# Optimization experiments

Hardware: AMD Instinct MI355X
Metric: run time of the kernel (lower is better)

Reference implementation:

```python
import jax, jax.numpy as jnp
import numpy as np

B, T, E = 2, 4096, 768
H = 12
WIN = 256  # one-sided window w; band width = 2w+1


def setup_inputs() -> dict:
    key = jax.random.key(0)
    k1, k2, k3, k4 = jax.random.split(key, 4)
    scale = 1.0 / np.sqrt(E)
    return {
        "x": jax.random.normal(k1, (B, T, E), dtype=jnp.float32),
        "Wq": jax.random.normal(k2, (E, E), dtype=jnp.float32) * scale,
        "Wk": jax.random.normal(k3, (E, E), dtype=jnp.float32) * scale,
        "Wv": jax.random.normal(k4, (E, E), dtype=jnp.float32) * scale,
    }


def reference(x, Wq, Wk, Wv):
    b, t, e = x.shape
    h, w = H, WIN
    s = e // h
    Wb = 2 * w + 1          # band width
    nc = t // w             # number of query chunks of size w

    # projections (nn.Linear, bias=False): y = x @ W^T
    q = (x @ Wq.T).reshape(b, t, h, s) * (1.0 / np.sqrt(s))
    k = (x @ Wk.T).reshape(b, t, h, s)
    v = (x @ Wv.T).reshape(b, t, h, s)

    # overlapping key/value chunks: chunk c covers absolute keys [c*w - w, c*w + 2w)
    pad = [(0, 0), (w, w), (0, 0), (0, 0)]
    kp = jnp.pad(k, pad).reshape(b, nc + 2, w, h, s)
    k3 = jnp.concatenate([kp[:, :-2], kp[:, 1:-1], kp[:, 2:]], axis=2)  # [b,nc,3w,h,s]
    vp = jnp.pad(v, pad).reshape(b, nc + 2, w, h, s)
    v3 = jnp.concatenate([vp[:, :-2], vp[:, 1:-1], vp[:, 2:]], axis=2)  # [b,nc,3w,h,s]

    qc = q.reshape(b, nc, w, h, s)
    scores = jnp.einsum('bcxhd,bcyhd->bhcxy', qc, k3)  # [b,h,nc,w,3w]

    # extract the banded diagonals: band j <-> key index p + j in the 3w window
    idx = jnp.arange(w)[:, None] + jnp.arange(Wb)[None, :]  # [w, 2w+1], values in [0,3w)
    band = jnp.take_along_axis(scores, idx[None, None, None], axis=-1)  # [b,h,nc,w,2w+1]
    band = band.reshape(b, h, t, Wb).transpose(0, 2, 1, 3)  # [b,t,h,2w+1]

    # mask_invalid_locations: key absolute pos = i + j - w must lie in [0, t)
    key_pos = jnp.arange(t)[:, None] + jnp.arange(Wb)[None, :] - w
    invalid = (key_pos < 0) | (key_pos >= t)
    band = jnp.where(invalid[None, :, None, :], -jnp.inf, band)

    probs = jax.nn.softmax(band.astype(jnp.float32), axis=-1).astype(x.dtype)

    # sliding_chunks_matmul_pv: scatter band probs back to the 3w window layout
    pc = probs.transpose(0, 2, 1, 3).reshape(b, h, nc, w, Wb)
    pc_pad = jnp.pad(pc, [(0, 0)] * 4 + [(w - 1, w - 1)])  # last axis len 4w-1
    # full[p, m] = band[p, m - p] for m-p in [0, 2w], else 0
    idx2 = (jnp.arange(3 * w)[None, :] - jnp.arange(w)[:, None]) + (w - 1)  # [w, 3w]
    pfull = jnp.take_along_axis(pc_pad, idx2[None, None, None], axis=-1)  # [b,h,nc,w,3w]

    out = jnp.einsum('bhcpm,bcmhd->bcphd', pfull, v3).reshape(b, t, e)
    return out
```

## Files before the change

kernel.cpp:

```cpp
#include <hip/hip_runtime.h>

#define B_ 2
#define T_ 4096
#define E_ 768
#define H_ 12
#define S_ 64
#define WIN_ 256

typedef unsigned short u16;
typedef unsigned int u32;
typedef __attribute__((ext_vector_type(8))) short bf16x8;
typedef __attribute__((ext_vector_type(4))) short bf16x4;
typedef __attribute__((ext_vector_type(4))) float f32x4;

__device__ __forceinline__ u16 f2bf(float f) {
  u32 u = __float_as_uint(f);
  u += ((u >> 16) & 1u) + 0x7fffu;
  return (u16)(u >> 16);
}

__device__ __forceinline__ u32 cvt_pk_bf16(float lo, float hi) {
  u32 r;
  asm("v_cvt_pk_bf16_f32 %0, %1, %2" : "=v"(r) : "v"(lo), "v"(hi));
  return r;
}

__device__ __forceinline__ void async_copy16(const u16* g, u16* l) {
  __builtin_amdgcn_global_load_lds(
      (const __attribute__((address_space(1))) void*)g,
      (__attribute__((address_space(3))) void*)l, 16, 0, 0);
}

__global__ void cvt_all(const float* __restrict__ x, const float* __restrict__ wq,
                        const float* __restrict__ wk, const float* __restrict__ wv,
                        u16* __restrict__ xb, u16* __restrict__ wb) {
  const int n4x = B_ * T_ * E_ / 4;
  const int n4w = E_ * E_ / 4;
  int i = blockIdx.x * 256 + threadIdx.x;
  const float* src;
  u16* dst;
  int j;
  if (i < n4x) {
    src = x; dst = xb; j = i;
  } else {
    int t = i - n4x;
    int z = t / n4w;
    if (z >= 3) return;
    j = t - z * n4w;
    src = (z == 0) ? wq : ((z == 1) ? wk : wv);
    dst = wb + (size_t)z * E_ * E_;
  }
  float4 v = ((const float4*)src)[j];
  ushort4 o;
  o.x = f2bf(v.x); o.y = f2bf(v.y); o.z = f2bf(v.z); o.w = f2bf(v.w);
  ((ushort4*)dst)[j] = o;
}

__global__ __launch_bounds__(256)
void gemm_qkv(const u16* __restrict__ xb, const u16* __restrict__ wb,
              u16* __restrict__ qkv) {
  const int M = B_ * T_;
  __shared__ u16 As[3][128][32];
  __shared__ u16 Bs[3][128][32];
  int tid = threadIdx.x;
  int lane = tid & 63, wave = tid >> 6;
  int wr = wave >> 1, wc = wave & 1;
  int q8 = lane >> 4, nl = lane & 15;
  int bm = blockIdx.x * 128, bn = blockIdx.y * 128;
  int z = blockIdx.z;
  const u16* A = xb;
  const u16* Bmat = wb + (size_t)z * E_ * E_;
  u16* C = qkv + (size_t)z * M * E_;
  float scale = (z == 0) ? (0.125f * 1.44269504088896f) : 1.0f;

  int r0 = tid >> 2, c0 = tid & 3;
  int cs = c0 ^ (r0 & 3);
  const u16* ga0 = A + (size_t)(bm + r0) * E_ + cs * 8;
  const u16* ga1 = A + (size_t)(bm + r0 + 64) * E_ + cs * 8;
  const u16* gb0 = Bmat + (size_t)(bn + r0) * E_ + cs * 8;
  const u16* gb1 = Bmat + (size_t)(bn + r0 + 64) * E_ + cs * 8;
  int l0 = tid * 8;
  int l1 = tid * 8 + 2048;

  int swz8 = (q8 ^ (nl & 3)) * 8;

  const int NK = E_ / 32;
#pragma unroll
  for (int p = 0; p < 2; ++p) {
    int koff = p * 32;
    async_copy16(ga0 + koff, &As[p][0][0] + l0);
    async_copy16(ga1 + koff, &As[p][0][0] + l1);
    async_copy16(gb0 + koff, &Bs[p][0][0] + l0);
    async_copy16(gb1 + koff, &Bs[p][0][0] + l1);
  }

  f32x4 acc[4][4] = {};

#define KSTEP(KI, BUF, PBUF)                                                   \
  {                                                                            \
    asm volatile("s_waitcnt vmcnt(4) lgkmcnt(0)" ::: "memory");                \
    __builtin_amdgcn_s_barrier();                                              \
    __builtin_amdgcn_sched_barrier(0);                                         \
    int kp = ((KI) + 2 < NK) ? (KI) + 2 : NK - 1;                              \
    int koff = kp * 32;                                                        \
    async_copy16(ga0 + koff, &As[PBUF][0][0] + l0);                            \
    async_copy16(ga1 + koff, &As[PBUF][0][0] + l1);                            \
    async_copy16(gb0 + koff, &Bs[PBUF][0][0] + l0);                            \
    async_copy16(gb1 + koff, &Bs[PBUF][0][0] + l1);                            \
    bf16x8 af[4], bfr[4];                                                      \
    _Pragma("unroll")                                                          \
    for (int i = 0; i < 4; ++i)                                                \
      af[i] = *(const bf16x8*)&As[BUF][wr * 64 + i * 16 + nl][swz8];           \
    _Pragma("unroll")                                                          \
    for (int i = 0; i < 4; ++i)                                                \
      bfr[i] = *(const bf16x8*)&Bs[BUF][wc * 64 + i * 16 + nl][swz8];          \
    __builtin_amdgcn_s_setprio(1);                                             \
    _Pragma("unroll")                                                          \
    for (int i = 0; i < 4; ++i)                                                \
      _Pragma("unroll")                                                        \
      for (int j2 = 0; j2 < 4; ++j2)                                           \
        acc[i][j2] = __builtin_amdgcn_mfma_f32_16x16x32_bf16(af[i], bfr[j2],   \
                                                             acc[i][j2], 0, 0, 0); \
    __builtin_amdgcn_s_setprio(0);                                             \
  }

  for (int kb = 0; kb < NK; kb += 3) {
    KSTEP(kb + 0, 0, 2)
    KSTEP(kb + 1, 1, 0)
    KSTEP(kb + 2, 2, 1)
  }
#undef KSTEP

#pragma unroll
  for (int i = 0; i < 4; ++i)
#pragma unroll
    for (int j2 = 0; j2 < 4; ++j2)
#pragma unroll
      for (int r = 0; r < 4; ++r) {
        int row = bm + wr * 64 + i * 16 + q8 * 4 + r;
        int col = bn + wc * 64 + j2 * 16 + nl;
        C[(size_t)row * E_ + col] = f2bf(acc[i][j2][r] * scale);
      }
}

__global__ void transpose_v(const u16* __restrict__ v, u16* __restrict__ vT) {
  __shared__ u16 lt[64][66];
  int t = threadIdx.x;
  int t0 = blockIdx.x * 64;
  int e0 = blockIdx.y * 64;
  int b = blockIdx.z;
#pragma unroll
  for (int i = 0; i < 2; ++i) {
    int u = t + i * 256;
    int tok = u >> 3, cg = u & 7;
    bf16x8 val = *(const bf16x8*)(v + (size_t)(b * T_ + t0 + tok) * E_ + e0 + cg * 8);
#pragma unroll
    for (int j = 0; j < 8; ++j) lt[tok][cg * 8 + j] = (u16)val[j];
  }
  __syncthreads();
#pragma unroll
  for (int i = 0; i < 2; ++i) {
    int u = t + i * 256;
    int d = u >> 3, ck = u & 7;
    bf16x8 o;
#pragma unroll
    for (int j = 0; j < 8; ++j) o[j] = (short)lt[ck * 8 + j][d];
    *(bf16x8*)(vT + (size_t)(b * E_ + e0 + d) * T_ + t0 + ck * 8) = o;
  }
}

__global__ __launch_bounds__(256)
void attn_kernel(const u16* __restrict__ qkv, const u16* __restrict__ vT,
                 float* __restrict__ out) {
  const int Mtot = B_ * T_;
  const u16* qb = qkv;
  const u16* kb = qkv + (size_t)Mtot * E_;

  int tid = threadIdx.x;
  int lane = tid & 63, wave = tid >> 6;
  int q8 = lane >> 4, nl = lane & 15;
  int qs = blockIdx.x * 128;
  int bh = blockIdx.y;
  int b = bh / H_, h = bh % H_;
  int qw = qs + wave * 32;
  size_t ho = (size_t)h * S_;

  bf16x8 aq[2][2];
#pragma unroll
  for (int mt = 0; mt < 2; ++mt) {
    const u16* qrow = qb + (size_t)(b * T_ + qw + mt * 16 + nl) * E_ + ho;
    aq[mt][0] = *(const bf16x8*)(qrow + q8 * 8);
    aq[mt][1] = *(const bf16x8*)(qrow + 32 + q8 * 8);
  }

  f32x4 O[2][4] = {};
  float lacc[2] = {0.f, 0.f};

  int klo = qw - WIN_; if (klo < 0) klo = 0;
  int khi = qw + 32 + WIN_; if (khi > T_) khi = T_;

  const u16* kbase = kb + (size_t)b * T_ * E_ + ho;
  const u16* vbase = vT + (size_t)b * E_ * T_ + ho * T_;

  int alo = ((((q8 << 1) & 3) << 4) + nl) << 2;
  int ahi = alo + 64;
  bool hint = q8 >= 2;

  bf16x8 bk[2][2];
#pragma unroll
  for (int nt = 0; nt < 2; ++nt) {
    const u16* krow = kbase + (size_t)(klo + nt * 16 + nl) * E_;
    bk[nt][0] = *(const bf16x8*)(krow + q8 * 8);
    bk[nt][1] = *(const bf16x8*)(krow + 32 + q8 * 8);
  }

  for (int kt = klo; kt < khi; kt += 32) {
    bf16x8 bv[4];
#pragma unroll
    for (int dt = 0; dt < 4; ++dt)
      bv[dt] = *(const bf16x8*)(vbase + (size_t)(dt * 16 + nl) * T_ + kt + q8 * 8);

    int ktn = (kt + 32 < khi) ? kt + 32 : kt;
    bf16x8 nbk[2][2];
#pragma unroll
    for (int nt = 0; nt < 2; ++nt) {
      const u16* krow = kbase + (size_t)(ktn + nt * 16 + nl) * E_;
      nbk[nt][0] = *(const bf16x8*)(krow + q8 * 8);
      nbk[nt][1] = *(const bf16x8*)(krow + 32 + q8 * 8);
    }

    f32x4 sc[2][2] = {};
    __builtin_amdgcn_s_setprio(1);
#pragma unroll
    for (int nt = 0; nt < 2; ++nt)
#pragma unroll
      for (int mt = 0; mt < 2; ++mt) {
        sc[mt][nt] = __builtin_amdgcn_mfma_f32_16x16x32_bf16(bk[nt][0], aq[mt][0], sc[mt][nt], 0, 0, 0);
        sc[mt][nt] = __builtin_amdgcn_mfma_f32_16x16x32_bf16(bk[nt][1], aq[mt][1], sc[mt][nt], 0, 0, 0);
      }
    __builtin_amdgcn_s_setprio(0);

    if (kt < qw - 225 || kt > qw + 225) {
#pragma unroll
      for (int mt = 0; mt < 2; ++mt)
#pragma unroll
        for (int nt = 0; nt < 2; ++nt)
#pragma unroll
          for (int r = 0; r < 4; ++r) {
            int qa = qw + mt * 16 + nl;
            int ka = kt + nt * 16 + q8 * 4 + r;
            int d = ka - qa;
            sc[mt][nt][r] = (d < -WIN_ || d > WIN_) ? -1e30f : sc[mt][nt][r];
          }
    }

#pragma unroll
    for (int mt = 0; mt < 2; ++mt) {
      float s = 0.f;
#pragma unroll
      for (int nt = 0; nt < 2; ++nt)
#pragma unroll
        for (int r = 0; r < 4; ++r) {
          float p = exp2f(sc[mt][nt][r]);
          sc[mt][nt][r] = p;
          s += p;
        }
      lacc[mt] += s;
    }

    bf16x8 ap[2];
#pragma unroll
    for (int mt = 0; mt < 2; ++mt) {
      u32 pk00 = cvt_pk_bf16(sc[mt][0][0], sc[mt][0][1]);
      u32 pk01 = cvt_pk_bf16(sc[mt][0][2], sc[mt][0][3]);
      u32 pk10 = cvt_pk_bf16(sc[mt][1][0], sc[mt][1][1]);
      u32 pk11 = cvt_pk_bf16(sc[mt][1][2], sc[mt][1][3]);
      int q0a = __builtin_amdgcn_ds_bpermute(alo, (int)pk00);
      int q0b = __builtin_amdgcn_ds_bpermute(alo, (int)pk10);
      int q1a = __builtin_amdgcn_ds_bpermute(alo, (int)pk01);
      int q1b = __builtin_amdgcn_ds_bpermute(alo, (int)pk11);
      int q2a = __builtin_amdgcn_ds_bpermute(ahi, (int)pk00);
      int q2b = __builtin_amdgcn_ds_bpermute(ahi, (int)pk10);
      int q3a = __builtin_amdgcn_ds_bpermute(ahi, (int)pk01);
      int q3b = __builtin_amdgcn_ds_bpermute(ahi, (int)pk11);
      union { u32 w[4]; bf16x8 v; } u;
      u.w[0] = (u32)(hint ? q0b : q0a);
      u.w[1] = (u32)(hint ? q1b : q1a);
      u.w[2] = (u32)(hint ? q2b : q2a);
      u.w[3] = (u32)(hint ? q3b : q3a);
      ap[mt] = u.v;
    }

    __builtin_amdgcn_s_setprio(1);
#pragma unroll
    for (int dt = 0; dt < 4; ++dt)
#pragma unroll
      for (int mt = 0; mt < 2; ++mt)
        O[mt][dt] = __builtin_amdgcn_mfma_f32_16x16x32_bf16(ap[mt], bv[dt], O[mt][dt], 0, 0, 0);
    __builtin_amdgcn_s_setprio(0);

#pragma unroll
    for (int nt = 0; nt < 2; ++nt) {
      bk[nt][0] = nbk[nt][0];
      bk[nt][1] = nbk[nt][1];
    }
  }

#pragma unroll
  for (int mt = 0; mt < 2; ++mt) {
    lacc[mt] += __shfl_xor(lacc[mt], 16);
    lacc[mt] += __shfl_xor(lacc[mt], 32);
  }

#pragma unroll
  for (int mt = 0; mt < 2; ++mt)
#pragma unroll
    for (int r = 0; r < 4; ++r) {
      float lq = __shfl(lacc[mt], (lane & 48) | (q8 * 4 + r));
      float inv = 1.0f / lq;
      int qa = qw + mt * 16 + q8 * 4 + r;
      float* op = out + (size_t)(b * T_ + qa) * E_ + ho;
#pragma unroll
      for (int dt = 0; dt < 4; ++dt)
        op[dt * 16 + nl] = O[mt][dt][r] * inv;
    }
}

extern "C" void kernel_launch(void* const* d_in, const int* in_sizes, int n_in,
                              void* d_out, int out_size, void* d_ws, size_t ws_size,
                              hipStream_t stream) {
  const float* x  = (const float*)d_in[0];
  const float* Wq = (const float*)d_in[1];
  const float* Wk = (const float*)d_in[2];
  const float* Wv = (const float*)d_in[3];
  float* out = (float*)d_out;

  const size_t M = (size_t)B_ * T_;
  u16* xb  = (u16*)d_ws;
  u16* wb  = xb + M * E_;
  u16* qkv = wb + 3 * (size_t)E_ * E_;
  u16* vT  = xb;

  const int n4x = B_ * T_ * E_ / 4;
  const int n4w = E_ * E_ / 4;
  int cvt_blocks = (n4x + 3 * n4w + 255) / 256;
  cvt_all<<<cvt_blocks, 256, 0, stream>>>(x, Wq, Wk, Wv, xb, wb);

  dim3 g1(M / 128, E_ / 128, 3);
  gemm_qkv<<<g1, 256, 0, stream>>>(xb, wb, qkv);

  dim3 gt(T_ / 64, E_ / 64, B_);
  transpose_v<<<gt, 256, 0, stream>>>(qkv + 2 * M * E_, vT);

  dim3 g2(T_ / 128, B_ * H_);
  attn_kernel<<<g2, 256, 0, stream>>>(qkv, vT, out);
}
```

Measured before the change: 185.6 us.

## Split attention key loop across wave pairs and remap blocks per XCD

Each 32-query tile is now handled by two waves that take alternating 32-key chunks, so the block grows to 512 threads. The two partial outputs and row sums are combined through shared memory before the final normalisation and store. Block indices are also remapped so that neighbouring query tiles of the same head land on the same XCD, which should improve L2 reuse of K/V. The aim is to double wave-level parallelism and shorten each wave's serial loop, at the cost of a reduction through LDS, a block-wide barrier, and higher per-block register and LDS demand.

```diff
diff --git a/kernel.cpp b/kernel.cpp
--- a/kernel.cpp
+++ b/kernel.cpp
@@ -6,6 +6,7 @@
 #define H_ 12
 #define S_ 64
 #define WIN_ 256
+#define GX_ 32
 
 typedef unsigned short u16;
 typedef unsigned int u32;
@@ -169,20 +170,28 @@
   }
 }
 
-__global__ __launch_bounds__(256)
+__global__ __launch_bounds__(512, 6)
 void attn_kernel(const u16* __restrict__ qkv, const u16* __restrict__ vT,
                  float* __restrict__ out) {
   const int Mtot = B_ * T_;
   const u16* qb = qkv;
   const u16* kb = qkv + (size_t)Mtot * E_;
 
+  __shared__ float cb[4][64][35];
+
   int tid = threadIdx.x;
   int lane = tid & 63, wave = tid >> 6;
+  int pair = wave >> 1;
+  int phase = wave & 1;
   int q8 = lane >> 4, nl = lane & 15;
-  int qs = blockIdx.x * 128;
-  int bh = blockIdx.y;
-  int b = bh / H_, h = bh % H_;
-  int qw = qs + wave * 32;
+
+  int d = blockIdx.y * GX_ + blockIdx.x;
+  int xcd = d & 7, j = d >> 3;
+  int nx = xcd * 4 + (j & 3);
+  int ny = j >> 2;
+  int qs = nx * 128;
+  int b = ny / H_, h = ny % H_;
+  int qw = qs + pair * 32;
   size_t ho = (size_t)h * S_;
 
   bf16x8 aq[2][2];
@@ -198,6 +207,7 @@
 
   int klo = qw - WIN_; if (klo < 0) klo = 0;
   int khi = qw + 32 + WIN_; if (khi > T_) khi = T_;
+  int kst = klo + phase * 32;
 
   const u16* kbase = kb + (size_t)b * T_ * E_ + ho;
   const u16* vbase = vT + (size_t)b * E_ * T_ + ho * T_;
@@ -209,18 +219,18 @@
   bf16x8 bk[2][2];
 #pragma unroll
   for (int nt = 0; nt < 2; ++nt) {
-    const u16* krow = kbase + (size_t)(klo + nt * 16 + nl) * E_;
+    const u16* krow = kbase + (size_t)(kst + nt * 16 + nl) * E_;
     bk[nt][0] = *(const bf16x8*)(krow + q8 * 8);
     bk[nt][1] = *(const bf16x8*)(krow + 32 + q8 * 8);
   }
 
-  for (int kt = klo; kt < khi; kt += 32) {
+  for (int kt = kst; kt < khi; kt += 64) {
     bf16x8 bv[4];
 #pragma unroll
     for (int dt = 0; dt < 4; ++dt)
       bv[dt] = *(const bf16x8*)(vbase + (size_t)(dt * 16 + nl) * T_ + kt + q8 * 8);
 
-    int ktn = (kt + 32 < khi) ? kt + 32 : kt;
+    int ktn = (kt + 64 < khi) ? kt + 64 : kt;
     bf16x8 nbk[2][2];
 #pragma unroll
     for (int nt = 0; nt < 2; ++nt) {
@@ -249,8 +259,8 @@
           for (int r = 0; r < 4; ++r) {
             int qa = qw + mt * 16 + nl;
             int ka = kt + nt * 16 + q8 * 4 + r;
-            int d = ka - qa;
-            sc[mt][nt][r] = (d < -WIN_ || d > WIN_) ? -1e30f : sc[mt][nt][r];
+            int dd = ka - qa;
+            sc[mt][nt][r] = (dd < -WIN_ || dd > WIN_) ? -1e30f : sc[mt][nt][r];
           }
     }
 
@@ -306,24 +316,48 @@
     }
   }
 
-#pragma unroll
-  for (int mt = 0; mt < 2; ++mt) {
-    lacc[mt] += __shfl_xor(lacc[mt], 16);
-    lacc[mt] += __shfl_xor(lacc[mt], 32);
-  }
-
-#pragma unroll
-  for (int mt = 0; mt < 2; ++mt)
-#pragma unroll
-    for (int r = 0; r < 4; ++r) {
-      float lq = __shfl(lacc[mt], (lane & 48) | (q8 * 4 + r));
-      float inv = 1.0f / lq;
-      int qa = qw + mt * 16 + q8 * 4 + r;
-      float* op = out + (size_t)(b * T_ + qa) * E_ + ho;
+  if (phase == 1) {
+    float* dst = &cb[pair][lane][0];
+#pragma unroll
+    for (int mt = 0; mt < 2; ++mt)
 #pragma unroll
       for (int dt = 0; dt < 4; ++dt)
-        op[dt * 16 + nl] = O[mt][dt][r] * inv;
-    }
+#pragma unroll
+        for (int r = 0; r < 4; ++r) dst[mt * 16 + dt * 4 + r] = O[mt][dt][r];
+    dst[32] = lacc[0];
+    dst[33] = lacc[1];
+  }
+  __syncthreads();
+  if (phase == 0) {
+    const float* src = &cb[pair][lane][0];
+#pragma unroll
+    for (int mt = 0; mt < 2; ++mt)
+#pragma unroll
+      for (int dt = 0; dt < 4; ++dt)
+#pragma unroll
+        for (int r = 0; r < 4; ++r) O[mt][dt][r] += src[mt * 16 + dt * 4 + r];
+    lacc[0] += src[32];
+    lacc[1] += src[33];
+
+#pragma unroll
+    for (int mt = 0; mt < 2; ++mt) {
+      lacc[mt] += __shfl_xor(lacc[mt], 16);
+      lacc[mt] += __shfl_xor(lacc[mt], 32);
+    }
+
+#pragma unroll
+    for (int mt = 0; mt < 2; ++mt)
+#pragma unroll
+      for (int r = 0; r < 4; ++r) {
+        float lq = __shfl(lacc[mt], (lane & 48) | (q8 * 4 + r));
+        float inv = 1.0f / lq;
+        int qa = qw + mt * 16 + q8 * 4 + r;
+        float* op = out + (size_t)(b * T_ + qa) * E_ + ho;
+#pragma unroll
+        for (int dt = 0; dt < 4; ++dt)
+          op[dt * 16 + nl] = O[mt][dt][r] * inv;
+      }
+  }
 }
 
 extern "C" void kernel_launch(void* const* d_in, const int* in_sizes, int n_in,
@@ -352,6 +386,6 @@
   dim3 gt(T_ / 64, E_ / 64, B_);
   transpose_v<<<gt, 256, 0, stream>>>(qkv + 2 * M * E_, vT);
 
-  dim3 g2(T_ / 128, B_ * H_);
-  attn_kernel<<<g2, 256, 0, stream>>>(qkv, vT, out);
-}
+  dim3 g2(GX_, B_ * H_);
+  attn_kernel<<<g2, 512, 0, stream>>>(qkv, vT, out);
+}
```

Measured after the change: 410.0 us. +120.9%, slower.

## Prefetch V tiles one step ahead, remap blocks per XCD, set occupancy bound

Applied to the files above, without the earlier changes.

The attention loop now loads the next V^T tile together with the next K tile, so V loads are double-buffered like K and their latency is hidden behind the current MFMAs. The block index is remapped so that groups of adjacent query tiles for the same head land on the same XCD, which should improve L2 reuse of overlapping K/V windows. A launch bound of 4 blocks per CU is added to limit register use. The extra prefetch registers could reduce occupancy or cause spills.

```diff
diff --git a/kernel.cpp b/kernel.cpp
--- a/kernel.cpp
+++ b/kernel.cpp
@@ -6,6 +6,7 @@
 #define H_ 12
 #define S_ 64
 #define WIN_ 256
+#define GX_ 32
 
 typedef unsigned short u16;
 typedef unsigned int u32;
@@ -169,7 +170,7 @@
   }
 }
 
-__global__ __launch_bounds__(256)
+__global__ __launch_bounds__(256, 4)
 void attn_kernel(const u16* __restrict__ qkv, const u16* __restrict__ vT,
                  float* __restrict__ out) {
   const int Mtot = B_ * T_;
@@ -179,9 +180,13 @@
   int tid = threadIdx.x;
   int lane = tid & 63, wave = tid >> 6;
   int q8 = lane >> 4, nl = lane & 15;
-  int qs = blockIdx.x * 128;
-  int bh = blockIdx.y;
-  int b = bh / H_, h = bh % H_;
+
+  int d = blockIdx.y * GX_ + blockIdx.x;
+  int xcd = d & 7, jj = d >> 3;
+  int nx = xcd * 4 + (jj & 3);
+  int ny = jj >> 2;
+  int qs = nx * 128;
+  int b = ny / H_, h = ny % H_;
   int qw = qs + wave * 32;
   size_t ho = (size_t)h * S_;
 
@@ -206,28 +211,29 @@
   int ahi = alo + 64;
   bool hint = q8 >= 2;
 
-  bf16x8 bk[2][2];
+  bf16x8 bk[2][2], bv[4];
 #pragma unroll
   for (int nt = 0; nt < 2; ++nt) {
     const u16* krow = kbase + (size_t)(klo + nt * 16 + nl) * E_;
     bk[nt][0] = *(const bf16x8*)(krow + q8 * 8);
     bk[nt][1] = *(const bf16x8*)(krow + 32 + q8 * 8);
   }
+#pragma unroll
+  for (int dt = 0; dt < 4; ++dt)
+    bv[dt] = *(const bf16x8*)(vbase + (size_t)(dt * 16 + nl) * T_ + klo + q8 * 8);
 
   for (int kt = klo; kt < khi; kt += 32) {
-    bf16x8 bv[4];
-#pragma unroll
-    for (int dt = 0; dt < 4; ++dt)
-      bv[dt] = *(const bf16x8*)(vbase + (size_t)(dt * 16 + nl) * T_ + kt + q8 * 8);
-
     int ktn = (kt + 32 < khi) ? kt + 32 : kt;
-    bf16x8 nbk[2][2];
+    bf16x8 nbk[2][2], nbv[4];
 #pragma unroll
     for (int nt = 0; nt < 2; ++nt) {
       const u16* krow = kbase + (size_t)(ktn + nt * 16 + nl) * E_;
       nbk[nt][0] = *(const bf16x8*)(krow + q8 * 8);
       nbk[nt][1] = *(const bf16x8*)(krow + 32 + q8 * 8);
     }
+#pragma unroll
+    for (int dt = 0; dt < 4; ++dt)
+      nbv[dt] = *(const bf16x8*)(vbase + (size_t)(dt * 16 + nl) * T_ + ktn + q8 * 8);
 
     f32x4 sc[2][2] = {};
     __builtin_amdgcn_s_setprio(1);
@@ -249,8 +255,8 @@
           for (int r = 0; r < 4; ++r) {
             int qa = qw + mt * 16 + nl;
             int ka = kt + nt * 16 + q8 * 4 + r;
-            int d = ka - qa;
-            sc[mt][nt][r] = (d < -WIN_ || d > WIN_) ? -1e30f : sc[mt][nt][r];
+            int dd = ka - qa;
+            sc[mt][nt][r] = (dd < -WIN_ || dd > WIN_) ? -1e30f : sc[mt][nt][r];
           }
     }
 
@@ -304,6 +310,8 @@
       bk[nt][0] = nbk[nt][0];
       bk[nt][1] = nbk[nt][1];
     }
+#pragma unroll
+    for (int dt = 0; dt < 4; ++dt) bv[dt] = nbv[dt];
   }
 
 #pragma unroll
@@ -352,6 +360,6 @@
   dim3 gt(T_ / 64, E_ / 64, B_);
   transpose_v<<<gt, 256, 0, stream>>>(qkv + 2 * M * E_, vT);
 
-  dim3 g2(T_ / 128, B_ * H_);
+  dim3 g2(GX_, B_ * H_);
   attn_kernel<<<g2, 256, 0, stream>>>(qkv, vT, out);
 }
```

Measured after the change: 273.5 us. 47.4% more time.
